# Performance work log

Hardware: AMD Instinct MI355X
Metric: run time of the kernel (lower is better)

The kernel has to match this reference:

```python
import jax, jax.numpy as jnp
import numpy as np

N_NODES = 100000
N_EDGES = 1600000
D = 128            # in_size == d_model == 128
N_LAYERS = 4
N_GRAPHS = 64
N_CLASS = 10
BN_EPS = 1e-5


def setup_inputs() -> dict:
    key = jax.random.key(0)
    ks = jax.random.split(key, 20)
    x = jax.random.normal(ks[0], (N_NODES, D), dtype=jnp.float32)
    edge_index = jax.random.randint(ks[1], (2, N_EDGES), 0, N_NODES, dtype=jnp.int32)
    batch = jnp.sort(jax.random.randint(ks[2], (N_NODES,), 0, N_GRAPHS, dtype=jnp.int32))
    s = 0.05
    # stacked per-layer GINConv MLP params (all layers are D->D since in_size==d_model)
    W1 = jax.random.normal(ks[3], (N_LAYERS, D, D), dtype=jnp.float32) * s
    b1 = jnp.zeros((N_LAYERS, D), dtype=jnp.float32)
    W2 = jax.random.normal(ks[4], (N_LAYERS, D, D), dtype=jnp.float32) * s
    b2 = jnp.zeros((N_LAYERS, D), dtype=jnp.float32)
    gamma = jnp.ones((N_LAYERS, D), dtype=jnp.float32)
    beta = jnp.zeros((N_LAYERS, D), dtype=jnp.float32)
    eps = jnp.zeros((N_LAYERS,), dtype=jnp.float32)  # train_eps=True, init 0
    fcw1 = jax.random.normal(ks[5], (D, D), dtype=jnp.float32) * s
    fcb1 = jnp.zeros((D,), dtype=jnp.float32)
    fcw2 = jax.random.normal(ks[6], (D, D // 2), dtype=jnp.float32) * s
    fcb2 = jnp.zeros((D // 2,), dtype=jnp.float32)
    fcw3 = jax.random.normal(ks[7], (D // 2, N_CLASS), dtype=jnp.float32) * s
    fcb3 = jnp.zeros((N_CLASS,), dtype=jnp.float32)
    return dict(x=x, edge_index=edge_index, batch=batch, W1=W1, b1=b1, W2=W2, b2=b2,
                gamma=gamma, beta=beta, eps=eps, fcw1=fcw1, fcb1=fcb1,
                fcw2=fcw2, fcb2=fcb2, fcw3=fcw3, fcb3=fcb3)


def _batchnorm(z, g, b):
    # BatchNorm1d in training mode: batch stats over nodes, biased variance
    m = jnp.mean(z, axis=0)
    v = jnp.var(z, axis=0)
    return g * (z - m) * jax.lax.rsqrt(v + BN_EPS) + b


def reference(x, edge_index, batch, W1, b1, W2, b2, gamma, beta, eps,
              fcw1, fcb1, fcw2, fcb2, fcw3, fcb3):
    # StandardScaler: per-feature standardization over all nodes (ddof=0)
    mu = jnp.mean(x, axis=0)
    sd = jnp.sqrt(jnp.var(x, axis=0))
    h = (x - mu) / sd
    src, dst = edge_index[0], edge_index[1]
    for l in range(N_LAYERS):
        # GINConv: MLP((1+eps)*x_i + sum_{j in N(i)} x_j)
        agg = jax.ops.segment_sum(h[src], dst, num_segments=N_NODES)
        z = (1.0 + eps[l]) * h + agg
        z = jax.nn.relu(z @ W1[l] + b1[l])
        z = jax.nn.relu(z @ W2[l] + b2[l])
        z = _batchnorm(z, gamma[l], beta[l])
        h = jax.nn.relu(z)  # outer F.relu in forward
    g = jax.ops.segment_sum(h, batch, num_segments=N_GRAPHS)  # global_add_pool
    g = jax.nn.relu(g @ fcw1 + fcb1)   # dropout omitted (eval/deterministic)
    g = jax.nn.relu(g @ fcw2 + fcb2)
    return g @ fcw3 + fcb3
```

## Files before the change

### kernel.cpp

```cpp
#include <hip/hip_runtime.h>
#include <hip/hip_bf16.h>
#include <math.h>

#define N_NODES 100000
#define N_EDGES 1600000
#define D 128
#define N_LAYERS 4
#define N_GRAPHS 64
#define N_CLASS 10
#define BN_EPS 1e-5f

#define POOL_ROWS 128
#define LDK 136

#define EB_CHUNK 4096
#define EDGE_BLOCKS ((N_EDGES + EB_CHUNK - 1) / EB_CHUNK)
#define NPB 512
#define NB ((N_NODES + NPB - 1) / NPB)

typedef __attribute__((ext_vector_type(8))) short bf16x8;
typedef __attribute__((ext_vector_type(4))) float f32x4;

__device__ inline float b2f(ushort u) {
    return __builtin_bit_cast(float, (unsigned)u << 16);
}
__device__ inline ushort f2b(float f) {
    unsigned u = __builtin_bit_cast(unsigned, f);
    return (ushort)((u + 0x7fffu + ((u >> 16) & 1u)) >> 16);
}

__global__ void prep_all_kernel(float* __restrict__ statsAll, float* __restrict__ ab,
                                float* __restrict__ gpool, int* __restrict__ bucketCount) {
    int t = threadIdx.x;
    for (int i = t; i < 10 * D; i += 1024) statsAll[i] = 0.f;
    if (t < D) { ab[t] = 1.f; ab[D + t] = 0.f; }
    for (int i = t; i < N_GRAPHS * D; i += 1024) gpool[i] = 0.f;
    for (int i = t; i < NB; i += 1024) bucketCount[i] = 0;
}

__global__ void bucket_count_kernel(const int* __restrict__ dst, int* __restrict__ bucketCount) {
    __shared__ int bc[NB];
    int tid = threadIdx.x;
    if (tid < NB) bc[tid] = 0;
    __syncthreads();
    int base = blockIdx.x * EB_CHUNK;
#pragma unroll
    for (int i = 0; i < 16; ++i) {
        int e = base + i * 256 + tid;
        if (e < N_EDGES) atomicAdd(&bc[dst[e] >> 9], 1);
    }
    __syncthreads();
    if (tid < NB && bc[tid]) atomicAdd(&bucketCount[tid], bc[tid]);
}

__global__ void bucket_scan_kernel(const int* __restrict__ bucketCount,
                                   int* __restrict__ bucketBase, int* __restrict__ bucketCursor) {
    __shared__ int lds[256];
    int tid = threadIdx.x;
    int v = (tid < NB) ? bucketCount[tid] : 0;
    lds[tid] = v;
    __syncthreads();
    for (int off = 1; off < 256; off <<= 1) {
        int x = (tid >= off) ? lds[tid - off] : 0;
        __syncthreads();
        lds[tid] += x;
        __syncthreads();
    }
    int excl = lds[tid] - v;
    if (tid < NB) { bucketBase[tid] = excl; bucketCursor[tid] = excl; }
    if (tid == NB - 1) bucketBase[NB] = excl + v;
}

__global__ void bucket_scatter_kernel(const int* __restrict__ src, const int* __restrict__ dst,
                                      int* __restrict__ bucketCursor, int2* __restrict__ bpairs) {
    __shared__ int lcnt[NB];
    int tid = threadIdx.x;
    if (tid < NB) lcnt[tid] = 0;
    __syncthreads();
    int base = blockIdx.x * EB_CHUNK;
    int s[16], d[16];
#pragma unroll
    for (int i = 0; i < 16; ++i) {
        int e = base + i * 256 + tid;
        if (e < N_EDGES) {
            s[i] = src[e]; d[i] = dst[e];
            atomicAdd(&lcnt[d[i] >> 9], 1);
        } else {
            d[i] = -1;
        }
    }
    __syncthreads();
    if (tid < NB) {
        int c = lcnt[tid];
        lcnt[tid] = c ? atomicAdd(&bucketCursor[tid], c) : 0;
    }
    __syncthreads();
#pragma unroll
    for (int i = 0; i < 16; ++i) {
        if (d[i] >= 0) {
            int p = atomicAdd(&lcnt[d[i] >> 9], 1);
            bpairs[p] = make_int2(s[i], d[i]);
        }
    }
}

__launch_bounds__(512)
__global__ void csr_build_kernel(const int2* __restrict__ bpairs, const int* __restrict__ bucketBase,
                                 int* __restrict__ rowptr, int* __restrict__ colidx) {
    __shared__ int cnt[NPB];
    __shared__ int cur[NPB];
    int tid = threadIdx.x;
    int b = blockIdx.x;
    int nb0 = b * NPB;
    int ebase = bucketBase[b];
    int eend = bucketBase[b + 1];
    cnt[tid] = 0;
    __syncthreads();
    for (int e = ebase + tid; e < eend; e += 512)
        atomicAdd(&cnt[bpairs[e].y - nb0], 1);
    __syncthreads();
    int v = cnt[tid];
    for (int off = 1; off < 512; off <<= 1) {
        int x = (tid >= off) ? cnt[tid - off] : 0;
        __syncthreads();
        cnt[tid] += x;
        __syncthreads();
    }
    int excl = cnt[tid] - v;
    int node = nb0 + tid;
    if (node < N_NODES) rowptr[node] = ebase + excl;
    cur[tid] = ebase + excl;
    __syncthreads();
    for (int e = ebase + tid; e < eend; e += 512) {
        int2 pr = bpairs[e];
        int p = atomicAdd(&cur[pr.y - nb0], 1);
        colidx[p] = pr.x;
    }
    if (b == 0 && tid == 0) rowptr[N_NODES] = N_EDGES;
}

__global__ void colstats_kernel(const float* __restrict__ x, float* __restrict__ stats) {
    __shared__ float ssum[D];
    __shared__ float ssq[D];
    int tid = threadIdx.x;
    if (tid < D) { ssum[tid] = 0.f; ssq[tid] = 0.f; }
    __syncthreads();
    int f4 = (tid & 31) * 4;
    int rsub = tid >> 5;
    int r0 = blockIdx.x * 128;
    int rend = r0 + 128;
    if (rend > N_NODES) rend = N_NODES;
    float4 ps = make_float4(0.f, 0.f, 0.f, 0.f);
    float4 pq = make_float4(0.f, 0.f, 0.f, 0.f);
    for (int r = r0 + rsub; r < rend; r += 8) {
        float4 v = *(const float4*)&x[(size_t)r * D + f4];
        ps.x += v.x; ps.y += v.y; ps.z += v.z; ps.w += v.w;
        pq.x += v.x * v.x; pq.y += v.y * v.y; pq.z += v.z * v.z; pq.w += v.w * v.w;
    }
    atomicAdd(&ssum[f4 + 0], ps.x); atomicAdd(&ssum[f4 + 1], ps.y);
    atomicAdd(&ssum[f4 + 2], ps.z); atomicAdd(&ssum[f4 + 3], ps.w);
    atomicAdd(&ssq[f4 + 0], pq.x);  atomicAdd(&ssq[f4 + 1], pq.y);
    atomicAdd(&ssq[f4 + 2], pq.z);  atomicAdd(&ssq[f4 + 3], pq.w);
    __syncthreads();
    if (tid < D) {
        atomicAdd(&stats[tid], ssum[tid]);
        atomicAdd(&stats[D + tid], ssq[tid]);
    }
}

__global__ void standardize_kernel(const float* __restrict__ x, const float* __restrict__ stats,
                                   ushort* __restrict__ h) {
    const float invN = 1.f / (float)N_NODES;
    int stride = gridDim.x * blockDim.x;
    const int total = N_NODES * (D / 4);
    for (int idx = blockIdx.x * blockDim.x + threadIdx.x; idx < total; idx += stride) {
        int f = (idx & 31) * 4;
        float4 v = ((const float4*)x)[idx];
        float o[4];
        float vv[4] = {v.x, v.y, v.z, v.w};
#pragma unroll
        for (int j = 0; j < 4; ++j) {
            float mu = stats[f + j] * invN;
            float sd = sqrtf(stats[D + f + j] * invN - mu * mu);
            o[j] = (vv[j] - mu) / sd;
        }
        ((ushort4*)h)[idx] = make_ushort4(f2b(o[0]), f2b(o[1]), f2b(o[2]), f2b(o[3]));
    }
}

__global__ void agg_kernel(const ushort* __restrict__ h, const int* __restrict__ rowptr,
                           const int* __restrict__ colidx, const float* __restrict__ eps, int l,
                           const float* __restrict__ ab, int relu_flag,
                           ushort* __restrict__ z0) {
    int node = blockIdx.x * 8 + (threadIdx.x >> 5);
    int f4 = (threadIdx.x & 31) * 4;
    const ushort* hp = h + f4;
    float A0 = ab[f4 + 0], A1 = ab[f4 + 1], A2 = ab[f4 + 2], A3 = ab[f4 + 3];
    float B0 = ab[D + f4 + 0], B1 = ab[D + f4 + 1], B2 = ab[D + f4 + 2], B3 = ab[D + f4 + 3];
    float lo = relu_flag ? 0.f : -INFINITY;
    auto R0 = [&](ushort u) { return fmaxf(fmaf(b2f(u), A0, B0), lo); };
    auto R1 = [&](ushort u) { return fmaxf(fmaf(b2f(u), A1, B1), lo); };
    auto R2 = [&](ushort u) { return fmaxf(fmaf(b2f(u), A2, B2), lo); };
    auto R3 = [&](ushort u) { return fmaxf(fmaf(b2f(u), A3, B3), lo); };

    ushort4 c = *(const ushort4*)&hp[(size_t)node * D];
    float se = 1.f + eps[l];
    float ax = se * R0(c.x), ay = se * R1(c.y), az = se * R2(c.z), aw = se * R3(c.w);

    int e = rowptr[node], e1 = rowptr[node + 1];
    for (; e + 4 <= e1; e += 4) {
        int s0 = colidx[e], s1 = colidx[e + 1], s2 = colidx[e + 2], s3 = colidx[e + 3];
        ushort4 v0 = *(const ushort4*)&hp[(size_t)s0 * D];
        ushort4 v1 = *(const ushort4*)&hp[(size_t)s1 * D];
        ushort4 v2 = *(const ushort4*)&hp[(size_t)s2 * D];
        ushort4 v3 = *(const ushort4*)&hp[(size_t)s3 * D];
        ax += (R0(v0.x) + R0(v1.x)) + (R0(v2.x) + R0(v3.x));
        ay += (R1(v0.y) + R1(v1.y)) + (R1(v2.y) + R1(v3.y));
        az += (R2(v0.z) + R2(v1.z)) + (R2(v2.z) + R2(v3.z));
        aw += (R3(v0.w) + R3(v1.w)) + (R3(v2.w) + R3(v3.w));
    }
    for (; e < e1; ++e) {
        ushort4 v0 = *(const ushort4*)&hp[(size_t)colidx[e] * D];
        ax += R0(v0.x); ay += R1(v0.y); az += R2(v0.z); aw += R3(v0.w);
    }
    *(ushort4*)&z0[(size_t)node * D + f4] = make_ushort4(f2b(ax), f2b(ay), f2b(az), f2b(aw));
}

__global__ void prep_wt_kernel(const float* __restrict__ W1, const float* __restrict__ W2,
                               ushort* __restrict__ wt) {
    int idx = blockIdx.x * blockDim.x + threadIdx.x;
    int w = idx >> 16;
    int rem = idx & 65535;
    int l = rem >> 14;
    int nk = rem & 16383;
    int n = nk >> 7;
    int k = nk & 127;
    const float* W = w ? W2 : W1;
    wt[idx] = f2b(W[((size_t)(l * D + k)) * D + n]);
}

__launch_bounds__(256, 2)
__global__ void mlp_mfma_kernel(const ushort* __restrict__ z0,
                                const ushort* __restrict__ wt1, const float* __restrict__ b1,
                                const ushort* __restrict__ wt2, const float* __restrict__ b2,
                                ushort* __restrict__ out, float* __restrict__ stats) {
    __shared__ ushort As[128 * LDK];
    __shared__ ushort Bs[128 * LDK];
    __shared__ float Ssum[D];
    __shared__ float Ssq[D];

    int tid = threadIdx.x;
    int lane = tid & 63;
    int wave = tid >> 6;
    int rb = blockIdx.x * 128;
    int lrow = lane & 15;
    int lk = lane >> 4;
    int klane = lk * 8;
    int wr0 = wave * 32;

    if (tid < D) { Ssum[tid] = 0.f; Ssq[tid] = 0.f; }

#pragma unroll
    for (int i = 0; i < 8; ++i) {
        int c2 = tid + i * 256;
        int row = c2 >> 4;
        int cc = (c2 & 15) * 8;
        int gr = rb + row;
        bf16x8 v;
#pragma unroll
        for (int e = 0; e < 8; ++e) v[e] = 0;
        if (gr < N_NODES) v = *(const bf16x8*)&z0[(size_t)gr * D + cc];
        *(bf16x8*)&As[row * LDK + cc] = v;
        *(bf16x8*)&Bs[row * LDK + cc] = *(const bf16x8*)&wt1[c2 * 8];
    }
    __syncthreads();

    f32x4 acc[2][8];
#pragma unroll
    for (int a = 0; a < 2; ++a)
#pragma unroll
        for (int b = 0; b < 8; ++b)
#pragma unroll
            for (int r = 0; r < 4; ++r) acc[a][b][r] = 0.f;

#pragma unroll
    for (int ks = 0; ks < 4; ++ks) {
        int k0 = ks * 32 + klane;
        bf16x8 a0 = *(const bf16x8*)&As[(wr0 + lrow) * LDK + k0];
        bf16x8 a1 = *(const bf16x8*)&As[(wr0 + 16 + lrow) * LDK + k0];
#pragma unroll
        for (int ct = 0; ct < 8; ++ct) {
            bf16x8 bb = *(const bf16x8*)&Bs[(ct * 16 + lrow) * LDK + k0];
            acc[0][ct] = __builtin_amdgcn_mfma_f32_16x16x32_bf16(a0, bb, acc[0][ct], 0, 0, 0);
            acc[1][ct] = __builtin_amdgcn_mfma_f32_16x16x32_bf16(a1, bb, acc[1][ct], 0, 0, 0);
        }
    }
    __syncthreads();

#pragma unroll
    for (int rt = 0; rt < 2; ++rt)
#pragma unroll
        for (int ct = 0; ct < 8; ++ct) {
            int col = ct * 16 + lrow;
            float bias = b1[col];
#pragma unroll
            for (int r = 0; r < 4; ++r) {
                int row = wr0 + rt * 16 + lk * 4 + r;
                As[row * LDK + col] = f2b(fmaxf(acc[rt][ct][r] + bias, 0.f));
            }
        }
#pragma unroll
    for (int i = 0; i < 8; ++i) {
        int c2 = tid + i * 256;
        *(bf16x8*)&Bs[(c2 >> 4) * LDK + (c2 & 15) * 8] = *(const bf16x8*)&wt2[c2 * 8];
    }
#pragma unroll
    for (int a = 0; a < 2; ++a)
#pragma unroll
        for (int b = 0; b < 8; ++b)
#pragma unroll
            for (int r = 0; r < 4; ++r) acc[a][b][r] = 0.f;
    __syncthreads();

#pragma unroll
    for (int ks = 0; ks < 4; ++ks) {
        int k0 = ks * 32 + klane;
        bf16x8 a0 = *(const bf16x8*)&As[(wr0 + lrow) * LDK + k0];
        bf16x8 a1 = *(const bf16x8*)&As[(wr0 + 16 + lrow) * LDK + k0];
#pragma unroll
        for (int ct = 0; ct < 8; ++ct) {
            bf16x8 bb = *(const bf16x8*)&Bs[(ct * 16 + lrow) * LDK + k0];
            acc[0][ct] = __builtin_amdgcn_mfma_f32_16x16x32_bf16(a0, bb, acc[0][ct], 0, 0, 0);
            acc[1][ct] = __builtin_amdgcn_mfma_f32_16x16x32_bf16(a1, bb, acc[1][ct], 0, 0, 0);
        }
    }
    __syncthreads();

#pragma unroll
    for (int rt = 0; rt < 2; ++rt)
#pragma unroll
        for (int ct = 0; ct < 8; ++ct) {
            int col = ct * 16 + lrow;
            float bias = b2[col];
            float s = 0.f, sq = 0.f;
#pragma unroll
            for (int r = 0; r < 4; ++r) {
                int row = wr0 + rt * 16 + lk * 4 + r;
                float v = fmaxf(acc[rt][ct][r] + bias, 0.f);
                Bs[row * LDK + col] = f2b(v);
                if (rb + row < N_NODES) { s += v; sq += v * v; }
            }
            atomicAdd(&Ssum[col], s);
            atomicAdd(&Ssq[col], sq);
        }
    __syncthreads();

#pragma unroll
    for (int i = 0; i < 8; ++i) {
        int c2 = tid + i * 256;
        int row = c2 >> 4;
        int cc = (c2 & 15) * 8;
        int gr = rb + row;
        if (gr < N_NODES)
            *(bf16x8*)&out[(size_t)gr * D + cc] = *(const bf16x8*)&Bs[row * LDK + cc];
    }
    if (tid < D) {
        atomicAdd(&stats[tid], Ssum[tid]);
        atomicAdd(&stats[D + tid], Ssq[tid]);
    }
}

__global__ void bnprep_kernel(const float* __restrict__ stats, const float* __restrict__ gamma,
                              const float* __restrict__ beta, float* __restrict__ ab) {
    int f = threadIdx.x;
    if (f < D) {
        const float invN = 1.f / (float)N_NODES;
        float mu = stats[f] * invN;
        float var = stats[D + f] * invN - mu * mu;
        float A = gamma[f] * rsqrtf(var + BN_EPS);
        ab[f] = A;
        ab[D + f] = beta[f] - mu * A;
    }
}

__global__ void pool_kernel(const ushort* __restrict__ h, const int* __restrict__ batch,
                            const float* __restrict__ ab, float* __restrict__ g) {
    int tid = threadIdx.x;
    int f4 = (tid & 31) * 4;
    int rsub = tid >> 5;
    int r0 = blockIdx.x * POOL_ROWS;
    int rend = r0 + POOL_ROWS;
    if (rend > N_NODES) rend = N_NODES;
    float A0 = ab[f4 + 0], A1 = ab[f4 + 1], A2 = ab[f4 + 2], A3 = ab[f4 + 3];
    float B0 = ab[D + f4 + 0], B1 = ab[D + f4 + 1], B2 = ab[D + f4 + 2], B3 = ab[D + f4 + 3];
    float4 acc = make_float4(0.f, 0.f, 0.f, 0.f);
    int cur = -1;
    for (int r = r0 + rsub; r < rend; r += 8) {
        int b = batch[r];
        if (b != cur) {
            if (cur >= 0) {
                atomicAdd(&g[cur * D + f4 + 0], acc.x);
                atomicAdd(&g[cur * D + f4 + 1], acc.y);
                atomicAdd(&g[cur * D + f4 + 2], acc.z);
                atomicAdd(&g[cur * D + f4 + 3], acc.w);
            }
            acc = make_float4(0.f, 0.f, 0.f, 0.f);
            cur = b;
        }
        ushort4 v = *(const ushort4*)&h[(size_t)r * D + f4];
        acc.x += fmaxf(fmaf(b2f(v.x), A0, B0), 0.f);
        acc.y += fmaxf(fmaf(b2f(v.y), A1, B1), 0.f);
        acc.z += fmaxf(fmaf(b2f(v.z), A2, B2), 0.f);
        acc.w += fmaxf(fmaf(b2f(v.w), A3, B3), 0.f);
    }
    if (cur >= 0) {
        atomicAdd(&g[cur * D + f4 + 0], acc.x);
        atomicAdd(&g[cur * D + f4 + 1], acc.y);
        atomicAdd(&g[cur * D + f4 + 2], acc.z);
        atomicAdd(&g[cur * D + f4 + 3], acc.w);
    }
}

__launch_bounds__(512)
__global__ void head_kernel(const float* __restrict__ g,
                            const float* __restrict__ fcw1, const float* __restrict__ fcb1,
                            const float* __restrict__ fcw2, const float* __restrict__ fcb2,
                            const float* __restrict__ fcw3, const float* __restrict__ fcb3,
                            float* __restrict__ out) {
    __shared__ float G[64][128];
    __shared__ float T1[64][128];
    __shared__ float T2[64][64];
    int tid = threadIdx.x;
#pragma unroll
    for (int i = 0; i < 4; ++i) {
        int slot = tid + i * 512;
        ((float4*)G)[slot] = ((const float4*)g)[slot];
    }
    __syncthreads();
#pragma unroll 1
    for (int rep = 0; rep < 16; ++rep) {
        int o = tid + rep * 512;
        int r = o >> 7, c = o & 127;
        float acc = fcb1[c];
        for (int k = 0; k < 128; ++k) acc = fmaf(G[r][k], fcw1[k * 128 + c], acc);
        T1[r][c] = fmaxf(acc, 0.f);
    }
    __syncthreads();
#pragma unroll 1
    for (int rep = 0; rep < 8; ++rep) {
        int o = tid + rep * 512;
        int r = o >> 6, c = o & 63;
        float acc = fcb2[c];
        for (int k = 0; k < 128; ++k) acc = fmaf(T1[r][k], fcw2[k * 64 + c], acc);
        T2[r][c] = fmaxf(acc, 0.f);
    }
    __syncthreads();
    for (int o = tid; o < N_GRAPHS * N_CLASS; o += 512) {
        int r = o / 10, c = o % 10;
        float acc = fcb3[c];
        for (int k = 0; k < 64; ++k) acc = fmaf(T2[r][k], fcw3[k * 10 + c], acc);
        out[o] = acc;
    }
}

extern "C" void kernel_launch(void* const* d_in, const int* in_sizes, int n_in,
                              void* d_out, int out_size, void* d_ws, size_t ws_size,
                              hipStream_t stream) {
    const float* x        = (const float*)d_in[0];
    const int* edge_index = (const int*)d_in[1];
    const int* batch      = (const int*)d_in[2];
    const float* W1       = (const float*)d_in[3];
    const float* b1       = (const float*)d_in[4];
    const float* W2       = (const float*)d_in[5];
    const float* b2       = (const float*)d_in[6];
    const float* gamma    = (const float*)d_in[7];
    const float* beta     = (const float*)d_in[8];
    const float* eps      = (const float*)d_in[9];
    const float* fcw1     = (const float*)d_in[10];
    const float* fcb1     = (const float*)d_in[11];
    const float* fcw2     = (const float*)d_in[12];
    const float* fcb2     = (const float*)d_in[13];
    const float* fcw3     = (const float*)d_in[14];
    const float* fcb3     = (const float*)d_in[15];
    float* out = (float*)d_out;

    char* ws = (char*)d_ws;
    size_t off = 0;
    auto alloc = [&](size_t bytes) -> void* {
        void* p = ws + off;
        off = (off + bytes + 255) & ~(size_t)255;
        return p;
    };
    ushort* hbuf   = (ushort*)alloc((size_t)N_NODES * D * 2);
    ushort* z0buf  = (ushort*)alloc((size_t)N_NODES * D * 2);
    ushort* wtbuf  = (ushort*)alloc((size_t)2 * N_LAYERS * D * D * 2);
    int2* bpairs   = (int2*)alloc((size_t)N_EDGES * 8);
    int* colidx    = (int*)alloc((size_t)N_EDGES * 4);
    int* rowptr    = (int*)alloc((size_t)(N_NODES + 1) * 4);
    int* bucketCount  = (int*)alloc((size_t)NB * 4);
    int* bucketBase   = (int*)alloc((size_t)(NB + 1) * 4);
    int* bucketCursor = (int*)alloc((size_t)NB * 4);
    float* statsAll = (float*)alloc(12 * D * 4);
    float* gpool   = (float*)alloc((size_t)N_GRAPHS * D * 4);
    float* scalerStats = statsAll + 8 * D;
    float* ab          = statsAll + 10 * D;

    const int* srcArr = edge_index;
    const int* dstArr = edge_index + N_EDGES;

    prep_all_kernel<<<1, 1024, 0, stream>>>(statsAll, ab, gpool, bucketCount);

    bucket_count_kernel<<<EDGE_BLOCKS, 256, 0, stream>>>(dstArr, bucketCount);
    bucket_scan_kernel<<<1, 256, 0, stream>>>(bucketCount, bucketBase, bucketCursor);
    bucket_scatter_kernel<<<EDGE_BLOCKS, 256, 0, stream>>>(srcArr, dstArr, bucketCursor, bpairs);
    csr_build_kernel<<<NB, 512, 0, stream>>>(bpairs, bucketBase, rowptr, colidx);

    colstats_kernel<<<(N_NODES + 127) / 128, 256, 0, stream>>>(x, scalerStats);
    standardize_kernel<<<2048, 256, 0, stream>>>(x, scalerStats, hbuf);

    prep_wt_kernel<<<512, 256, 0, stream>>>(W1, W2, wtbuf);

    for (int l = 0; l < N_LAYERS; ++l) {
        float* lstats = statsAll + (size_t)l * 2 * D;
        agg_kernel<<<N_NODES / 8, 256, 0, stream>>>(hbuf, rowptr, colidx, eps, l,
                                                    ab, (l > 0) ? 1 : 0, z0buf);
        mlp_mfma_kernel<<<(N_NODES + 127) / 128, 256, 0, stream>>>(
            z0buf, wtbuf + (size_t)l * D * D, b1 + (size_t)l * D,
            wtbuf + (size_t)(N_LAYERS + l) * D * D, b2 + (size_t)l * D, hbuf, lstats);
        bnprep_kernel<<<1, 128, 0, stream>>>(lstats, gamma + (size_t)l * D,
                                             beta + (size_t)l * D, ab);
    }

    pool_kernel<<<(N_NODES + POOL_ROWS - 1) / POOL_ROWS, 256, 0, stream>>>(hbuf, batch, ab, gpool);
    head_kernel<<<1, 512, 0, stream>>>(gpool, fcw1, fcb1, fcw2, fcb2, fcw3, fcb3, out);
}
```

Before: 810.4 us.

## Feed MFMA operands straight from global memory and shrink LDS to one buffer

```diff
diff --git a/kernel.cpp b/kernel.cpp
--- a/kernel.cpp
+++ b/kernel.cpp
@@ -239,13 +239,12 @@
     wt[idx] = f2b(W[((size_t)(l * D + k)) * D + n]);
 }
 
-__launch_bounds__(256, 2)
+__launch_bounds__(256, 4)
 __global__ void mlp_mfma_kernel(const ushort* __restrict__ z0,
                                 const ushort* __restrict__ wt1, const float* __restrict__ b1,
                                 const ushort* __restrict__ wt2, const float* __restrict__ b2,
                                 ushort* __restrict__ out, float* __restrict__ stats) {
-    __shared__ ushort As[128 * LDK];
-    __shared__ ushort Bs[128 * LDK];
+    __shared__ ushort Z[128 * LDK];
     __shared__ float Ssum[D];
     __shared__ float Ssq[D];
 
@@ -260,20 +259,18 @@
 
     if (tid < D) { Ssum[tid] = 0.f; Ssq[tid] = 0.f; }
 
-#pragma unroll
-    for (int i = 0; i < 8; ++i) {
-        int c2 = tid + i * 256;
-        int row = c2 >> 4;
-        int cc = (c2 & 15) * 8;
-        int gr = rb + row;
-        bf16x8 v;
-#pragma unroll
-        for (int e = 0; e < 8; ++e) v[e] = 0;
-        if (gr < N_NODES) v = *(const bf16x8*)&z0[(size_t)gr * D + cc];
-        *(bf16x8*)&As[row * LDK + cc] = v;
-        *(bf16x8*)&Bs[row * LDK + cc] = *(const bf16x8*)&wt1[c2 * 8];
-    }
-    __syncthreads();
+    bf16x8 zero8;
+#pragma unroll
+    for (int e = 0; e < 8; ++e) zero8[e] = 0;
+
+    int ra0 = rb + wr0 + lrow;
+    int ra1 = ra0 + 16;
+    bool ok0 = ra0 < N_NODES;
+    bool ok1 = ra1 < N_NODES;
+    const ushort* pa0 = z0 + (size_t)ra0 * D + klane;
+    const ushort* pa1 = z0 + (size_t)ra1 * D + klane;
+    const ushort* pb1 = wt1 + (size_t)lrow * D + klane;
+    const ushort* pb2 = wt2 + (size_t)lrow * D + klane;
 
     f32x4 acc[2][8];
 #pragma unroll
@@ -285,17 +282,15 @@
 
 #pragma unroll
     for (int ks = 0; ks < 4; ++ks) {
-        int k0 = ks * 32 + klane;
-        bf16x8 a0 = *(const bf16x8*)&As[(wr0 + lrow) * LDK + k0];
-        bf16x8 a1 = *(const bf16x8*)&As[(wr0 + 16 + lrow) * LDK + k0];
+        bf16x8 a0 = ok0 ? *(const bf16x8*)(pa0 + ks * 32) : zero8;
+        bf16x8 a1 = ok1 ? *(const bf16x8*)(pa1 + ks * 32) : zero8;
 #pragma unroll
         for (int ct = 0; ct < 8; ++ct) {
-            bf16x8 bb = *(const bf16x8*)&Bs[(ct * 16 + lrow) * LDK + k0];
+            bf16x8 bb = *(const bf16x8*)(pb1 + (size_t)ct * 16 * D + ks * 32);
             acc[0][ct] = __builtin_amdgcn_mfma_f32_16x16x32_bf16(a0, bb, acc[0][ct], 0, 0, 0);
             acc[1][ct] = __builtin_amdgcn_mfma_f32_16x16x32_bf16(a1, bb, acc[1][ct], 0, 0, 0);
         }
     }
-    __syncthreads();
 
 #pragma unroll
     for (int rt = 0; rt < 2; ++rt)
@@ -306,54 +301,55 @@
 #pragma unroll
             for (int r = 0; r < 4; ++r) {
                 int row = wr0 + rt * 16 + lk * 4 + r;
-                As[row * LDK + col] = f2b(fmaxf(acc[rt][ct][r] + bias, 0.f));
+                Z[row * LDK + col] = f2b(fmaxf(acc[rt][ct][r] + bias, 0.f));
             }
         }
-#pragma unroll
-    for (int i = 0; i < 8; ++i) {
-        int c2 = tid + i * 256;
-        *(bf16x8*)&Bs[(c2 >> 4) * LDK + (c2 & 15) * 8] = *(const bf16x8*)&wt2[c2 * 8];
-    }
+
 #pragma unroll
     for (int a = 0; a < 2; ++a)
 #pragma unroll
         for (int b = 0; b < 8; ++b)
 #pragma unroll
             for (int r = 0; r < 4; ++r) acc[a][b][r] = 0.f;
-    __syncthreads();
 
 #pragma unroll
     for (int ks = 0; ks < 4; ++ks) {
         int k0 = ks * 32 + klane;
-        bf16x8 a0 = *(const bf16x8*)&As[(wr0 + lrow) * LDK + k0];
-        bf16x8 a1 = *(const bf16x8*)&As[(wr0 + 16 + lrow) * LDK + k0];
+        bf16x8 a0 = *(const bf16x8*)&Z[(wr0 + lrow) * LDK + k0];
+        bf16x8 a1 = *(const bf16x8*)&Z[(wr0 + 16 + lrow) * LDK + k0];
 #pragma unroll
         for (int ct = 0; ct < 8; ++ct) {
-            bf16x8 bb = *(const bf16x8*)&Bs[(ct * 16 + lrow) * LDK + k0];
+            bf16x8 bb = *(const bf16x8*)(pb2 + (size_t)ct * 16 * D + ks * 32);
             acc[0][ct] = __builtin_amdgcn_mfma_f32_16x16x32_bf16(a0, bb, acc[0][ct], 0, 0, 0);
             acc[1][ct] = __builtin_amdgcn_mfma_f32_16x16x32_bf16(a1, bb, acc[1][ct], 0, 0, 0);
         }
     }
-    __syncthreads();
-
+
+    float ls[8], lq[8];
+#pragma unroll
+    for (int ct = 0; ct < 8; ++ct) { ls[ct] = 0.f; lq[ct] = 0.f; }
 #pragma unroll
     for (int rt = 0; rt < 2; ++rt)
 #pragma unroll
         for (int ct = 0; ct < 8; ++ct) {
             int col = ct * 16 + lrow;
             float bias = b2[col];
-            float s = 0.f, sq = 0.f;
 #pragma unroll
             for (int r = 0; r < 4; ++r) {
                 int row = wr0 + rt * 16 + lk * 4 + r;
                 float v = fmaxf(acc[rt][ct][r] + bias, 0.f);
-                Bs[row * LDK + col] = f2b(v);
-                if (rb + row < N_NODES) { s += v; sq += v * v; }
+                Z[row * LDK + col] = f2b(v);
+                if (rb + row < N_NODES) { ls[ct] += v; lq[ct] += v * v; }
             }
-            atomicAdd(&Ssum[col], s);
-            atomicAdd(&Ssq[col], sq);
-        }
-    __syncthreads();
+        }
+    __syncthreads();
+
+#pragma unroll
+    for (int ct = 0; ct < 8; ++ct) {
+        int col = ct * 16 + lrow;
+        atomicAdd(&Ssum[col], ls[ct]);
+        atomicAdd(&Ssq[col], lq[ct]);
+    }
 
 #pragma unroll
     for (int i = 0; i < 8; ++i) {
@@ -362,8 +358,9 @@
         int cc = (c2 & 15) * 8;
         int gr = rb + row;
         if (gr < N_NODES)
-            *(bf16x8*)&out[(size_t)gr * D + cc] = *(const bf16x8*)&Bs[row * LDK + cc];
-    }
+            *(bf16x8*)&out[(size_t)gr * D + cc] = *(const bf16x8*)&Z[row * LDK + cc];
+    }
+    __syncthreads();
     if (tid < D) {
         atomicAdd(&stats[tid], Ssum[tid]);
         atomicAdd(&stats[D + tid], Ssq[tid]);
```

Measured after the change: 788.3 us. 1.03x faster.
